# Kernel optimization log

Hardware: AMD Instinct MI355X
Metric: run time of the kernel (lower is better)

## Reference

```python
import jax, jax.numpy as jnp
import numpy as np

D_MODEL = 2048
NUM_HEADS = 16
HEAD_DIM = D_MODEL // NUM_HEADS  # 128
WINDOW = 1024
BATCH = 2
SEQ = 2048
NEG_INF = -1e9


def setup_inputs() -> dict:
    key = jax.random.key(0)
    ks = jax.random.split(key, 6)
    x = jax.random.normal(ks[0], (BATCH, SEQ, D_MODEL), dtype=jnp.float32)
    # RoPE frequencies (llama-style, theta=10000)
    inv_freq = 1.0 / (10000.0 ** (jnp.arange(0, HEAD_DIM, 2, dtype=jnp.float32) / HEAD_DIM))
    angles = jnp.arange(SEQ, dtype=jnp.float32)[:, None] * inv_freq[None, :]  # [S, hd/2]
    freqs_cos = jnp.cos(angles)
    freqs_sin = jnp.sin(angles)
    # additive causal mask [S, S]
    i = jnp.arange(SEQ)[:, None]
    j = jnp.arange(SEQ)[None, :]
    mask = jnp.where(j <= i, 0.0, NEG_INF).astype(jnp.float32)
    scale = 1.0 / np.sqrt(D_MODEL)
    w_q = jax.random.normal(ks[1], (D_MODEL, D_MODEL), dtype=jnp.float32) * scale
    w_k = jax.random.normal(ks[2], (D_MODEL, D_MODEL), dtype=jnp.float32) * scale
    w_v = jax.random.normal(ks[3], (D_MODEL, D_MODEL), dtype=jnp.float32) * scale
    w_o = jax.random.normal(ks[4], (D_MODEL, D_MODEL), dtype=jnp.float32) * scale
    return {"x": x, "freqs_cos": freqs_cos, "freqs_sin": freqs_sin, "mask": mask,
            "w_q": w_q, "w_k": w_k, "w_v": w_v, "w_o": w_o}


def _apply_rope(t, cos, sin):
    # t: [B, S, H, hd]; cos/sin: [S, hd/2]. Pairwise complex rotation.
    B, S, H, hd = t.shape
    tr = t.reshape(B, S, H, hd // 2, 2)
    a, b = tr[..., 0], tr[..., 1]
    c = cos[None, :, None, :]
    s = sin[None, :, None, :]
    out = jnp.stack([a * c - b * s, a * s + b * c], axis=-1)
    return out.reshape(B, S, H, hd)


def reference(x, freqs_cos, freqs_sin, mask, w_q, w_k, w_v, w_o):
    B, S, D = x.shape
    H, hd = NUM_HEADS, HEAD_DIM
    xq = (x @ w_q).reshape(B, S, H, hd)
    xk = (x @ w_k).reshape(B, S, H, hd)
    xv = (x @ w_v).reshape(B, S, H, hd)
    xq = _apply_rope(xq, freqs_cos, freqs_sin)
    xk = _apply_rope(xk, freqs_cos, freqs_sin)
    # scores: [B, H, S, S]
    scores = jnp.einsum("bqhd,bkhd->bhqk", xq, xk) / jnp.sqrt(jnp.asarray(hd, x.dtype))
    scores = scores + mask[None, None, :, :]
    # sliding-window mask: attend only to positions within WINDOW behind query
    i = jnp.arange(S)[:, None]
    j = jnp.arange(S)[None, :]
    sliding = (i - j >= 0) & (i - j < WINDOW)
    scores = jnp.where(sliding[None, None], scores, NEG_INF)
    probs = jax.nn.softmax(scores, axis=-1).astype(xq.dtype)
    out = jnp.einsum("bhqk,bkhd->bqhd", probs, xv).reshape(B, S, D)
    return out @ w_o
```

## Files before the change

### kernel.cpp

```cpp
#include <hip/hip_runtime.h>
#include <hip/hip_bf16.h>

typedef __attribute__((ext_vector_type(8))) short bf16x8;
typedef __attribute__((ext_vector_type(4))) float f32x4;
typedef unsigned short u16;
typedef unsigned int u32;

#define SEQ 2048
#define DMODEL 2048
#define NH 16
#define HD 128
#define NBATCH 2
#define WINDOW 1024

__device__ __forceinline__ float bf2f(u16 v) {
    union { u32 u; float f; } x; x.u = ((u32)v) << 16; return x.f;
}
__device__ __forceinline__ u16 f2bf(float f) {
    union { float f; u32 u; } x; x.f = f;
    u32 u = x.u;
    u32 r = (u + 0x7fffu + ((u >> 16) & 1u)) >> 16;
    return (u16)r;
}

__global__ __launch_bounds__(256) void cvt_f32_bf16(
    const float* __restrict__ in, u16* __restrict__ out)
{
    long i = ((long)blockIdx.x * 256 + threadIdx.x) * 8;
    float4 a = *(const float4*)(in + i);
    float4 b = *(const float4*)(in + i + 4);
    u16 v[8] = {f2bf(a.x), f2bf(a.y), f2bf(a.z), f2bf(a.w),
                f2bf(b.x), f2bf(b.y), f2bf(b.z), f2bf(b.w)};
    *(uint4*)(out + i) = *(uint4*)v;
}

__global__ __launch_bounds__(256) void transpose_f32_bf16(
    const float* __restrict__ in, u16* __restrict__ out, int R, int C)
{
    __shared__ u16 tile[64 * 72];
    const int c0 = blockIdx.x * 64, r0 = blockIdx.y * 64;
    const int t = threadIdx.x;
#pragma unroll
    for (int i = 0; i < 4; ++i) {
        int ch = i * 256 + t;
        int r = ch >> 4, c4 = (ch & 15) * 4;
        float4 v = *(const float4*)(in + (long)(r0 + r) * C + c0 + c4);
        tile[r * 72 + c4 + 0] = f2bf(v.x);
        tile[r * 72 + c4 + 1] = f2bf(v.y);
        tile[r * 72 + c4 + 2] = f2bf(v.z);
        tile[r * 72 + c4 + 3] = f2bf(v.w);
    }
    __syncthreads();
#pragma unroll
    for (int i = 0; i < 4; ++i) {
        int ch = i * 256 + t;
        int oc = ch >> 4, sg = (ch & 15) * 4;
        u16 vals[4];
#pragma unroll
        for (int j = 0; j < 4; ++j) vals[j] = tile[(sg + j) * 72 + oc];
        *(uint2*)(out + (long)(c0 + oc) * R + r0 + sg) = *(uint2*)vals;
    }
}

#define GLD16(gp, lp) __builtin_amdgcn_global_load_lds( \
    (const __attribute__((address_space(1))) u32*)(gp), \
    (__attribute__((address_space(3))) u32*)(lp), 16, 0, 0)
#define BAR() __builtin_amdgcn_s_barrier()
#define WAITV(n) asm volatile("s_waitcnt vmcnt(" #n ")" ::: "memory")

template <int MODE>
__global__ __launch_bounds__(512, 2) void gemm256(
    const u16* __restrict__ A, const u16* __restrict__ Bt,
    u16* __restrict__ OutB, float* __restrict__ OutF,
    const float* __restrict__ cosb, const float* __restrict__ sinb)
{
    extern __shared__ u16 sm[];
    const int t = threadIdx.x;
    const int w = t >> 6, l = t & 63;
    const int g = l >> 4, l15 = l & 15;
    const int wr = w >> 2, wc = w & 3;

    const int NWG = (MODE == 1) ? 384 : 128;
    const int cpx = NWG / 8;
    int bid = blockIdx.x;
    int wg = (bid & 7) * cpx + (bid >> 3);
    int z, m_t, n_t;
    if (MODE == 1) { z = wg >> 7; int rem = wg & 127; n_t = rem >> 4; m_t = rem & 15; }
    else           { z = 0; n_t = wg >> 4; m_t = wg & 15; }
    const int m0 = m_t * 256, n0 = n_t * 256;
    const u16* Ab = A + (long)m0 * 2048;
    const u16* Bb = Bt + (long)z * (2048L * 2048) + (long)n0 * 2048;

    const int lrow0 = t >> 3;
    const int kk16  = (t & 7) ^ (lrow0 & 7);
    const long a_g0 = (long)lrow0 * 2048 + kk16 * 8;
    const long b_g0 = (long)(((lrow0 >> 5) << 6) + (lrow0 & 31)) * 2048 + kk16 * 8;
    const int lds_w = w * 512;
    const int sw    = (l15 & 7) << 3;

#define STAGE_A(h, kt1) do { int _b = (kt1) & 1; \
    const u16* _gp = Ab + (long)(h) * (128 * 2048) + (long)(kt1) * 64 + a_g0; \
    u16* _lp = sm + (_b * 2 + (h)) * 8192 + lds_w; \
    GLD16(_gp, _lp); GLD16(_gp + 64 * 2048, _lp + 4096); } while (0)

#define STAGE_B(s, kt1) do { int _b = (kt1) & 1; \
    const u16* _gp = Bb + (long)(s) * (32 * 2048) + (long)(kt1) * 64 + b_g0; \
    u16* _lp = sm + 32768 + (_b * 2 + (s)) * 8192 + lds_w; \
    GLD16(_gp, _lp); GLD16(_gp + 128 * 2048, _lp + 4096); } while (0)

    bf16x8 af[4][2], bfr[2][2];
    f32x4 acc[8][4] = {};

#define LDA(mh, buf) { const u16* _ba = sm + ((buf) * 2 + wr) * 8192; \
    _Pragma("unroll") for (int i = 0; i < 4; ++i) { \
        int row = (mh) * 64 + i * 16 + l15; \
        _Pragma("unroll") for (int kx = 0; kx < 2; ++kx) \
            af[i][kx] = *(const bf16x8*)(_ba + row * 64 + ((kx * 32 + g * 8) ^ sw)); } }

#define LDB(q, buf) { const u16* _bb = sm + 32768 + ((buf) * 2 + (q)) * 8192; \
    _Pragma("unroll") for (int j = 0; j < 2; ++j) { \
        int row = wc * 32 + j * 16 + l15; \
        _Pragma("unroll") for (int kx = 0; kx < 2; ++kx) \
            bfr[j][kx] = *(const bf16x8*)(_bb + row * 64 + ((kx * 32 + g * 8) ^ sw)); } }

#define MM(mh, q) { __builtin_amdgcn_s_setprio(1); \
    _Pragma("unroll") for (int i = 0; i < 4; ++i) \
    _Pragma("unroll") for (int j = 0; j < 2; ++j) \
    _Pragma("unroll") for (int kx = 0; kx < 2; ++kx) \
        acc[(mh) * 4 + i][(q) * 2 + j] = __builtin_amdgcn_mfma_f32_16x16x32_bf16( \
            af[i][kx], bfr[j][kx], acc[(mh) * 4 + i][(q) * 2 + j], 0, 0, 0); \
    __builtin_amdgcn_s_setprio(0); }

    STAGE_A(0, 0); STAGE_A(1, 0); STAGE_B(0, 0); STAGE_B(1, 0);
    WAITV(2); BAR();

#pragma unroll 1
    for (int kt = 0; kt < 32; ++kt) {
        const int buf = kt & 1;
        const bool pf = (kt + 1 < 32);
        LDA(0, buf); LDB(0, buf);
        if (pf) { STAGE_A(0, kt + 1); WAITV(2); } else { WAITV(0); }
        BAR(); MM(0, 0); BAR();
        LDB(1, buf);
        if (pf) STAGE_A(1, kt + 1);
        BAR(); MM(0, 1); BAR();
        LDA(1, buf);
        if (pf) STAGE_B(0, kt + 1);
        BAR(); MM(1, 1); BAR();
        LDB(0, buf);
        if (pf) { STAGE_B(1, kt + 1); WAITV(2); }
        BAR(); MM(1, 0); BAR();
    }

#pragma unroll
    for (int mt = 0; mt < 8; ++mt) {
#pragma unroll
        for (int nt = 0; nt < 4; ++nt) {
#pragma unroll
            for (int r = 0; r < 4; ++r) {
                int m = m0 + wr * 128 + mt * 16 + g * 4 + r;
                int n = n0 + wc * 64 + nt * 16 + l15;
                float v = acc[mt][nt][r];
                if (MODE == 0) {
                    OutF[(long)m * 2048 + n] = v;
                } else {
                    int b = m >> 11, s = m & 2047;
                    int h = n >> 7,  d = n & 127;
                    float pv = __shfl_xor(v, 1);
                    if (z < 2) {
                        int p = d >> 1;
                        float cc = cosb[s * 64 + p];
                        float ss = sinb[s * 64 + p];
                        v = ((d & 1) == 0) ? (v * cc - pv * ss) : (pv * ss + v * cc);
                    }
                    long zoff = (long)z * (NBATCH * NH * SEQ * HD);
                    if (z == 2)
                        OutB[zoff + ((long)(b * NH + h) * HD + d) * SEQ + s] = f2bf(v);
                    else
                        OutB[zoff + ((long)(b * NH + h) * SEQ + s) * HD + d] = f2bf(v);
                }
            }
        }
    }
#undef STAGE_A
#undef STAGE_B
#undef LDA
#undef LDB
#undef MM
}

__global__ __launch_bounds__(256, 2) void attn_kernel(
    const u16* __restrict__ Q,
    const u16* __restrict__ K,
    const u16* __restrict__ Vt,
    u16* __restrict__ Out)
{
    __shared__ u16 k_lds[64 * 136];
    __shared__ u16 vt_lds[128 * 72];
    __shared__ u16 p_lds[4 * 16 * 72];
    const int t = threadIdx.x, w = t >> 6, l = t & 63;
    const int g = l >> 4, l15 = l & 15;
    const int q0 = blockIdx.x * 64;
    const int bh = blockIdx.y;
    const int qbase = q0 + w * 16;
    const u16* Qb = Q + (long)bh * SEQ * HD;
    const u16* Kb = K + (long)bh * SEQ * HD;
    const u16* Vb = Vt + (long)bh * HD * SEQ;
    u16* pw = p_lds + w * 16 * 72;

    bf16x8 qf[4];
#pragma unroll
    for (int kk = 0; kk < 4; ++kk)
        qf[kk] = *(const bf16x8*)(Qb + (long)(qbase + l15) * HD + kk * 32 + g * 8);

    f32x4 of[8] = {};
    float mrow[4] = {-1e30f, -1e30f, -1e30f, -1e30f};
    float lrow[4] = {0.f, 0.f, 0.f, 0.f};
    const float scale = 0.088388347648318447f;

    const int t0 = (q0 >= WINDOW) ? ((q0 - (WINDOW - 1)) >> 6) : 0;
    const int t1 = q0 >> 6;

    for (int kt = t0; kt <= t1; ++kt) {
        const int kv0 = kt * 64;
#pragma unroll
        for (int i = 0; i < 4; ++i) {
            int ch = i * 256 + t;
            { int r = ch >> 4, c = (ch & 15) * 8;
              *(uint4*)(k_lds + r * 136 + c) = *(const uint4*)(Kb + (long)(kv0 + r) * HD + c); }
            { int r = ch >> 3, c = (ch & 7) * 8;
              *(uint4*)(vt_lds + r * 72 + c) = *(const uint4*)(Vb + (long)r * SEQ + kv0 + c); }
        }
        __syncthreads();

        f32x4 sf[4] = {};
#pragma unroll
        for (int kk = 0; kk < 4; ++kk) {
#pragma unroll
            for (int nt = 0; nt < 4; ++nt) {
                bf16x8 kf = *(const bf16x8*)(k_lds + (nt * 16 + l15) * 136 + kk * 32 + g * 8);
                sf[nt] = __builtin_amdgcn_mfma_f32_16x16x32_bf16(qf[kk], kf, sf[nt], 0, 0, 0);
            }
        }
        const bool full = (kv0 + 63 <= qbase) && ((qbase + 15) - kv0 < WINDOW);
#pragma unroll
        for (int nt = 0; nt < 4; ++nt)
#pragma unroll
            for (int r = 0; r < 4; ++r) {
                float s = sf[nt][r] * scale;
                if (!full) {
                    int q = qbase + g * 4 + r;
                    int kv = kv0 + nt * 16 + l15;
                    bool ok = (kv <= q) && (q - kv < WINDOW);
                    s = ok ? s : -1e30f;
                }
                sf[nt][r] = s;
            }
        float fr[4];
#pragma unroll
        for (int r = 0; r < 4; ++r) {
            float v = fmaxf(fmaxf(sf[0][r], sf[1][r]), fmaxf(sf[2][r], sf[3][r]));
            v = fmaxf(v, __shfl_xor(v, 1));
            v = fmaxf(v, __shfl_xor(v, 2));
            v = fmaxf(v, __shfl_xor(v, 4));
            v = fmaxf(v, __shfl_xor(v, 8));
            float mn = fmaxf(mrow[r], v);
            fr[r] = __expf(mrow[r] - mn);
            mrow[r] = mn;
        }
        float rs[4] = {0.f, 0.f, 0.f, 0.f};
#pragma unroll
        for (int nt = 0; nt < 4; ++nt)
#pragma unroll
            for (int r = 0; r < 4; ++r) {
                float p = __expf(sf[nt][r] - mrow[r]);
                rs[r] += p;
                pw[(g * 4 + r) * 72 + nt * 16 + l15] = f2bf(p);
            }
#pragma unroll
        for (int r = 0; r < 4; ++r) {
            float v = rs[r];
            v += __shfl_xor(v, 1);
            v += __shfl_xor(v, 2);
            v += __shfl_xor(v, 4);
            v += __shfl_xor(v, 8);
            lrow[r] = lrow[r] * fr[r] + v;
        }
#pragma unroll
        for (int nd = 0; nd < 8; ++nd)
#pragma unroll
            for (int r = 0; r < 4; ++r) of[nd][r] *= fr[r];
#pragma unroll
        for (int kk = 0; kk < 2; ++kk) {
            bf16x8 pa = *(const bf16x8*)(pw + l15 * 72 + kk * 32 + g * 8);
#pragma unroll
            for (int nd = 0; nd < 8; ++nd) {
                bf16x8 vb = *(const bf16x8*)(vt_lds + (nd * 16 + l15) * 72 + kk * 32 + g * 8);
                of[nd] = __builtin_amdgcn_mfma_f32_16x16x32_bf16(pa, vb, of[nd], 0, 0, 0);
            }
        }
        __syncthreads();
    }
    const int b = bh >> 4, h = bh & 15;
#pragma unroll
    for (int r = 0; r < 4; ++r) {
        float inv = 1.0f / lrow[r];
        int q = qbase + g * 4 + r;
        u16* orow = Out + ((long)(b * SEQ + q)) * DMODEL + h * HD;
#pragma unroll
        for (int nd = 0; nd < 8; ++nd)
            orow[nd * 16 + l15] = f2bf(of[nd][r] * inv);
    }
}

extern "C" void kernel_launch(void* const* d_in, const int* in_sizes, int n_in,
                              void* d_out, int out_size, void* d_ws, size_t ws_size,
                              hipStream_t stream) {
    (void)in_sizes; (void)n_in; (void)out_size; (void)ws_size;
    const float* x    = (const float*)d_in[0];
    const float* fcos = (const float*)d_in[1];
    const float* fsin = (const float*)d_in[2];
    const float* wq = (const float*)d_in[4];
    const float* wk = (const float*)d_in[5];
    const float* wv = (const float*)d_in[6];
    const float* wo = (const float*)d_in[7];

    u16* ws = (u16*)d_ws;
    const long WT = 2048L * 2048;
    u16* xb  = ws;
    u16* wtq = xb + 8388608L;
    u16* wtk = wtq + WT;
    u16* wtv = wtk + WT;
    u16* wto = wtv + WT;
    u16* qkv = wto + WT;
    u16* q_ws = qkv;
    u16* k_ws = qkv + 8388608L;
    u16* vt_ws = qkv + 16777216L;
    u16* attn_ws = qkv + 25165824L;

    hipFuncSetAttribute(reinterpret_cast<const void*>(gemm256<1>),
                        hipFuncAttributeMaxDynamicSharedMemorySize, 131072);
    hipFuncSetAttribute(reinterpret_cast<const void*>(gemm256<0>),
                        hipFuncAttributeMaxDynamicSharedMemorySize, 131072);

    dim3 blk(256);
    cvt_f32_bf16<<<4096, blk, 0, stream>>>(x, xb);
    transpose_f32_bf16<<<dim3(32, 32), blk, 0, stream>>>(wq, wtq, 2048, 2048);
    transpose_f32_bf16<<<dim3(32, 32), blk, 0, stream>>>(wk, wtk, 2048, 2048);
    transpose_f32_bf16<<<dim3(32, 32), blk, 0, stream>>>(wv, wtv, 2048, 2048);
    transpose_f32_bf16<<<dim3(32, 32), blk, 0, stream>>>(wo, wto, 2048, 2048);
    gemm256<1><<<384, 512, 131072, stream>>>(xb, wtq, qkv, nullptr, fcos, fsin);
    attn_kernel<<<dim3(32, 32), blk, 0, stream>>>(q_ws, k_ws, vt_ws, attn_ws);
    gemm256<0><<<128, 512, 131072, stream>>>(attn_ws, wto, nullptr, (float*)d_out,
                                             nullptr, nullptr);
}
```

Before: 498.7 us.

## Shrink GEMM tile to 256x128 with triple-buffered LDS pipeline

Changes the GEMM block tile from 256x256 to 256x128, with the 8 waves arranged as 4x2, which doubles the grid for both the QKV and output projections. The goal is to fill all CUs and cut wave-quantization tails: the output GEMM previously ran 128 blocks. The k-loop moves from double buffering with four sub-phases to a triple-buffered LDS ring that prefetches two tiles ahead, with fewer barriers per iteration. In exchange, each block reuses less data per byte loaded and needs more LDS (144 KB), so it still runs one block per CU.

```diff
diff --git a/kernel.cpp b/kernel.cpp
--- a/kernel.cpp
+++ b/kernel.cpp
@@ -78,87 +78,85 @@
     const int t = threadIdx.x;
     const int w = t >> 6, l = t & 63;
     const int g = l >> 4, l15 = l & 15;
-    const int wr = w >> 2, wc = w & 3;
-
-    const int NWG = (MODE == 1) ? 384 : 128;
+    const int wr = w >> 1, wc = w & 1;
+
+    const int NWG = (MODE == 1) ? 768 : 256;
     const int cpx = NWG / 8;
     int bid = blockIdx.x;
     int wg = (bid & 7) * cpx + (bid >> 3);
     int z, m_t, n_t;
-    if (MODE == 1) { z = wg >> 7; int rem = wg & 127; n_t = rem >> 4; m_t = rem & 15; }
+    if (MODE == 1) { z = wg >> 8; int rem = wg & 255; n_t = rem >> 4; m_t = rem & 15; }
     else           { z = 0; n_t = wg >> 4; m_t = wg & 15; }
-    const int m0 = m_t * 256, n0 = n_t * 256;
+    const int m0 = m_t * 256, n0 = n_t * 128;
     const u16* Ab = A + (long)m0 * 2048;
     const u16* Bb = Bt + (long)z * (2048L * 2048) + (long)n0 * 2048;
 
-    const int lrow0 = t >> 3;
-    const int kk16  = (t & 7) ^ (lrow0 & 7);
-    const long a_g0 = (long)lrow0 * 2048 + kk16 * 8;
-    const long b_g0 = (long)(((lrow0 >> 5) << 6) + (lrow0 & 31)) * 2048 + kk16 * 8;
-    const int lds_w = w * 512;
-    const int sw    = (l15 & 7) << 3;
-
-#define STAGE_A(h, kt1) do { int _b = (kt1) & 1; \
-    const u16* _gp = Ab + (long)(h) * (128 * 2048) + (long)(kt1) * 64 + a_g0; \
-    u16* _lp = sm + (_b * 2 + (h)) * 8192 + lds_w; \
-    GLD16(_gp, _lp); GLD16(_gp + 64 * 2048, _lp + 4096); } while (0)
-
-#define STAGE_B(s, kt1) do { int _b = (kt1) & 1; \
-    const u16* _gp = Bb + (long)(s) * (32 * 2048) + (long)(kt1) * 64 + b_g0; \
-    u16* _lp = sm + 32768 + (_b * 2 + (s)) * 8192 + lds_w; \
-    GLD16(_gp, _lp); GLD16(_gp + 128 * 2048, _lp + 4096); } while (0)
+    const int r0 = t >> 3;
+    const int kk16 = (t & 7) ^ (r0 & 7);
+    const long g_off = (long)r0 * 2048 + kk16 * 8;
+    const int lds_l = w * 512;
+    const int sw = (l15 & 7) << 3;
+
+#define STAGE(bufS_, ktS_) do { \
+    const u16* _ga = Ab + (long)(ktS_) * 64 + g_off; \
+    u16* _la = sm + (bufS_) * 24576 + lds_l; \
+    GLD16(_ga,              _la); \
+    GLD16(_ga +  64 * 2048, _la + 4096); \
+    GLD16(_ga + 128 * 2048, _la + 8192); \
+    GLD16(_ga + 192 * 2048, _la + 12288); \
+    const u16* _gb = Bb + (long)(ktS_) * 64 + g_off; \
+    u16* _lb = sm + (bufS_) * 24576 + 16384 + lds_l; \
+    GLD16(_gb,              _lb); \
+    GLD16(_gb + 64 * 2048,  _lb + 4096); \
+} while (0)
 
     bf16x8 af[4][2], bfr[2][2];
-    f32x4 acc[8][4] = {};
-
-#define LDA(mh, buf) { const u16* _ba = sm + ((buf) * 2 + wr) * 8192; \
+    f32x4 acc[4][4] = {};
+
+#define LDA_ALL(bufv) { const u16* _ba = sm + (bufv) * 24576; \
     _Pragma("unroll") for (int i = 0; i < 4; ++i) { \
-        int row = (mh) * 64 + i * 16 + l15; \
+        int row = wr * 64 + i * 16 + l15; \
         _Pragma("unroll") for (int kx = 0; kx < 2; ++kx) \
             af[i][kx] = *(const bf16x8*)(_ba + row * 64 + ((kx * 32 + g * 8) ^ sw)); } }
 
-#define LDB(q, buf) { const u16* _bb = sm + 32768 + ((buf) * 2 + (q)) * 8192; \
+#define LDB_H(q, bufv) { const u16* _bb = sm + (bufv) * 24576 + 16384; \
     _Pragma("unroll") for (int j = 0; j < 2; ++j) { \
-        int row = wc * 32 + j * 16 + l15; \
+        int row = wc * 64 + (q) * 32 + j * 16 + l15; \
         _Pragma("unroll") for (int kx = 0; kx < 2; ++kx) \
             bfr[j][kx] = *(const bf16x8*)(_bb + row * 64 + ((kx * 32 + g * 8) ^ sw)); } }
 
-#define MM(mh, q) { __builtin_amdgcn_s_setprio(1); \
+#define MM(q) { __builtin_amdgcn_s_setprio(1); \
     _Pragma("unroll") for (int i = 0; i < 4; ++i) \
     _Pragma("unroll") for (int j = 0; j < 2; ++j) \
     _Pragma("unroll") for (int kx = 0; kx < 2; ++kx) \
-        acc[(mh) * 4 + i][(q) * 2 + j] = __builtin_amdgcn_mfma_f32_16x16x32_bf16( \
-            af[i][kx], bfr[j][kx], acc[(mh) * 4 + i][(q) * 2 + j], 0, 0, 0); \
+        acc[i][(q) * 2 + j] = __builtin_amdgcn_mfma_f32_16x16x32_bf16( \
+            af[i][kx], bfr[j][kx], acc[i][(q) * 2 + j], 0, 0, 0); \
     __builtin_amdgcn_s_setprio(0); }
 
-    STAGE_A(0, 0); STAGE_A(1, 0); STAGE_B(0, 0); STAGE_B(1, 0);
-    WAITV(2); BAR();
-
+    STAGE(0, 0); STAGE(1, 1);
+    WAITV(6); BAR();
+
+    int buf = 0, bufS = 2;
 #pragma unroll 1
     for (int kt = 0; kt < 32; ++kt) {
-        const int buf = kt & 1;
-        const bool pf = (kt + 1 < 32);
-        LDA(0, buf); LDB(0, buf);
-        if (pf) { STAGE_A(0, kt + 1); WAITV(2); } else { WAITV(0); }
-        BAR(); MM(0, 0); BAR();
-        LDB(1, buf);
-        if (pf) STAGE_A(1, kt + 1);
-        BAR(); MM(0, 1); BAR();
-        LDA(1, buf);
-        if (pf) STAGE_B(0, kt + 1);
-        BAR(); MM(1, 1); BAR();
-        LDB(0, buf);
-        if (pf) { STAGE_B(1, kt + 1); WAITV(2); }
-        BAR(); MM(1, 0); BAR();
-    }
-
-#pragma unroll
-    for (int mt = 0; mt < 8; ++mt) {
+        const int ktS = (kt + 2 <= 31) ? (kt + 2) : 31;
+        LDA_ALL(buf); LDB_H(0, buf);
+        STAGE(bufS, ktS);
+        BAR(); MM(0); BAR();
+        LDB_H(1, buf);
+        WAITV(6);
+        BAR(); MM(1); BAR();
+        buf  = (buf  == 2) ? 0 : buf + 1;
+        bufS = (bufS == 2) ? 0 : bufS + 1;
+    }
+
+#pragma unroll
+    for (int mt = 0; mt < 4; ++mt) {
 #pragma unroll
         for (int nt = 0; nt < 4; ++nt) {
 #pragma unroll
             for (int r = 0; r < 4; ++r) {
-                int m = m0 + wr * 128 + mt * 16 + g * 4 + r;
+                int m = m0 + wr * 64 + mt * 16 + g * 4 + r;
                 int n = n0 + wc * 64 + nt * 16 + l15;
                 float v = acc[mt][nt][r];
                 if (MODE == 0) {
@@ -182,10 +180,9 @@
             }
         }
     }
-#undef STAGE_A
-#undef STAGE_B
-#undef LDA
-#undef LDB
+#undef STAGE
+#undef LDA_ALL
+#undef LDB_H
 #undef MM
 }
 
@@ -339,9 +336,9 @@
     u16* attn_ws = qkv + 25165824L;
 
     hipFuncSetAttribute(reinterpret_cast<const void*>(gemm256<1>),
-                        hipFuncAttributeMaxDynamicSharedMemorySize, 131072);
+                        hipFuncAttributeMaxDynamicSharedMemorySize, 147456);
     hipFuncSetAttribute(reinterpret_cast<const void*>(gemm256<0>),
-                        hipFuncAttributeMaxDynamicSharedMemorySize, 131072);
+                        hipFuncAttributeMaxDynamicSharedMemorySize, 147456);
 
     dim3 blk(256);
     cvt_f32_bf16<<<4096, blk, 0, stream>>>(x, xb);
@@ -349,8 +346,8 @@
     transpose_f32_bf16<<<dim3(32, 32), blk, 0, stream>>>(wk, wtk, 2048, 2048);
     transpose_f32_bf16<<<dim3(32, 32), blk, 0, stream>>>(wv, wtv, 2048, 2048);
     transpose_f32_bf16<<<dim3(32, 32), blk, 0, stream>>>(wo, wto, 2048, 2048);
-    gemm256<1><<<384, 512, 131072, stream>>>(xb, wtq, qkv, nullptr, fcos, fsin);
+    gemm256<1><<<768, 512, 147456, stream>>>(xb, wtq, qkv, nullptr, fcos, fsin);
     attn_kernel<<<dim3(32, 32), blk, 0, stream>>>(q_ws, k_ws, vt_ws, attn_ws);
-    gemm256<0><<<128, 512, 131072, stream>>>(attn_ws, wto, nullptr, (float*)d_out,
+    gemm256<0><<<256, 512, 147456, stream>>>(attn_ws, wto, nullptr, (float*)d_out,
                                              nullptr, nullptr);
 }
```

Result: faster. 449.6 us (-9.9%).
